# Kernel tuning notes

Hardware: AMD Instinct MI355X
Metric: run time of the kernel (lower is better)

The kernel has to match this reference:

```python
import jax, jax.numpy as jnp
import numpy as np

B, C_IN, C_HID, H, W = 4, 512, 512, 64, 64


def setup_inputs() -> dict:
    key = jax.random.key(0)
    ks = jax.random.split(key, 9)
    s_in = 1.0 / np.sqrt(C_IN)
    s_hid = 1.0 / np.sqrt(C_HID)
    return {
        "inp": jax.random.normal(ks[0], (B, C_IN, H, W), dtype=jnp.float32),
        "Wk": jax.random.normal(ks[1], (C_HID, C_IN), dtype=jnp.float32) * s_in,
        "bk": jax.random.normal(ks[2], (C_HID,), dtype=jnp.float32) * 0.01,
        "Wq": jax.random.normal(ks[3], (C_HID, C_IN), dtype=jnp.float32) * s_in,
        "bq": jax.random.normal(ks[4], (C_HID,), dtype=jnp.float32) * 0.01,
        "Wv": jax.random.normal(ks[5], (C_HID, C_IN), dtype=jnp.float32) * s_in,
        "bv": jax.random.normal(ks[6], (C_HID,), dtype=jnp.float32) * 0.01,
        "Wo": jax.random.normal(ks[7], (C_IN, C_HID), dtype=jnp.float32) * s_hid,
        "bo": jax.random.normal(ks[8], (C_IN,), dtype=jnp.float32) * 0.01,
    }


def reference(inp, Wk, bk, Wq, bq, Wv, bv, Wo, bo):
    b, _, h, w = inp.shape
    n = h * w

    def conv1x1(x, Wt, bias):  # 1x1 conv == per-pixel GEMM
        return jnp.einsum('bchw,oc->bohw', x, Wt) + bias[None, :, None, None]

    k = conv1x1(inp, Wk, bk).reshape(b, C_HID, n)   # [B,Ch,N]
    q = conv1x1(inp, Wq, bq).reshape(b, C_HID, n)
    v = conv1x1(inp, Wv, bv).reshape(b, C_HID, n)

    scale = 1.0 / jnp.sqrt(jnp.asarray(C_HID, dtype=jnp.float32))
    # weight[b,i,j] = <key_i, query_j> / sqrt(Ch); softmax over j (dim=2)
    scores = jnp.einsum('bci,bcj->bij', k, q) * scale  # [B,N,N]
    weight = jax.nn.softmax(scores, axis=2)
    # out[b,c,i] = sum_j weight[b,i,j] * v[b,c,j]
    out = jnp.einsum('bij,bcj->bci', weight, v).reshape(b, C_HID, h, w)
    return conv1x1(out, Wo, bo)  # [B,C_in,H,W]
```

## Files before the change

### kernel.cpp

```cpp
#include <hip/hip_runtime.h>
#include <hip/hip_bf16.h>


typedef __attribute__((ext_vector_type(4))) float f32x4;
typedef __attribute__((ext_vector_type(8))) short short8;
typedef __attribute__((ext_vector_type(4))) short short4v;

#define QSCALE 0.06376639774f
#define FENCE asm volatile("" ::: "memory")
#define SBAR  do { FENCE; __builtin_amdgcn_s_barrier(); FENCE; } while (0)
#define LGKM0 asm volatile("s_waitcnt lgkmcnt(0)" ::: "memory")

__device__ __forceinline__ unsigned short f2bf(float f) {
  unsigned u = __builtin_bit_cast(unsigned, f);
  unsigned r = (u + 0x7FFFu + ((u >> 16) & 1u)) >> 16;
  return (unsigned short)r;
}

__device__ __forceinline__ void gll16(const void* g, void* l) {
  __builtin_amdgcn_global_load_lds((const __attribute__((address_space(1))) void*)g,
                                   (__attribute__((address_space(3))) void*)l, 16, 0, 0);
}

#define MFMA_BF16(d, va, vb) \
  d = __builtin_amdgcn_mfma_f32_16x16x32_bf16(va, vb, d, 0, 0, 0)

__device__ __forceinline__ void gemm256_fine(
    const short* __restrict__ A, int lda,
    const short* __restrict__ B, int ldb,
    int nkt, char* sm, f32x4 (&acc)[8][4]) {
  const int tid = threadIdx.x, w = tid >> 6, lane = tid & 63;
  const int g = lane >> 4, l15 = lane & 15;
  const int wm = w >> 2, wn = w & 3;
  const int swz = (l15 & 7) << 4;
  const int brow = (wn & 1) << 6;
  const char* SAb = sm + (wm << 14);
  const char* SBb = sm + 65536 + ((wn >> 1) << 14);

  auto stage = [&](int mat, int half, int t) {
    if (t >= nkt) return;
    char* dst = sm + mat * 65536 + ((t & 1) << 15) + (half << 14) + (w << 10);
    const short* src = mat ? B : A;
    const int ld = mat ? ldb : lda;
    const char* gs = (const char*)src + ((size_t)(half * 128) * ld + (size_t)t * 64) * 2;
#pragma unroll
    for (int q = 0; q < 2; ++q) {
      int o = (q << 13) | (w << 10) | (lane << 4);
      int row = o >> 7, cb = (o & 127) ^ ((row & 7) << 4);
      gll16(gs + (size_t)row * (ld * 2) + cb, dst + (q << 13));
    }
  };
  auto rdA = [&](short8* a4, int mf0, int ks, int buf) {
    const char* SA = SAb + (buf << 15);
#pragma unroll
    for (int i = 0; i < 4; ++i)
      a4[i] = *(const short8*)(SA + ((mf0 + i) * 16 + l15) * 128 + ((ks * 64 + g * 16) ^ swz));
  };
  auto rdB = [&](short8* b4, int ks, int buf) {
    const char* SB = SBb + (buf << 15);
#pragma unroll
    for (int nf = 0; nf < 4; ++nf)
      b4[nf] = *(const short8*)(SB + (brow + nf * 16 + l15) * 128 + ((ks * 64 + g * 16) ^ swz));
  };
  auto mm = [&](short8* a4, short8* b4, int mf0) {
    __builtin_amdgcn_s_setprio(1);
#pragma unroll
    for (int i = 0; i < 4; ++i)
#pragma unroll
      for (int nf = 0; nf < 4; ++nf)
        MFMA_BF16(acc[mf0 + i][nf], a4[i], b4[nf]);
    __builtin_amdgcn_s_setprio(0);
  };

  stage(1, 0, 0); stage(1, 1, 0); stage(0, 0, 0); stage(0, 1, 0); stage(1, 0, 1);

  for (int T = 0; T < nkt; T += 2) {
    short8 a[8], bb[4];
    asm volatile("s_waitcnt vmcnt(2)" ::: "memory"); SBAR;
    rdA(a, 0, 0, 0); rdB(bb, 0, 0); stage(1, 1, T + 1);
    SBAR; LGKM0; mm(a, bb, 0); SBAR;
    rdA(a + 4, 4, 0, 0); stage(0, 0, T + 1);
    SBAR; LGKM0; mm(a + 4, bb, 4); SBAR;
    rdA(a, 0, 1, 0); rdB(bb, 1, 0); stage(0, 1, T + 1);
    SBAR; LGKM0; mm(a, bb, 0); SBAR;
    rdA(a + 4, 4, 1, 0); stage(1, 0, T + 2);
    SBAR; LGKM0; mm(a + 4, bb, 4); SBAR;
    if (T + 2 < nkt) { asm volatile("s_waitcnt vmcnt(2)" ::: "memory"); }
    else             { asm volatile("s_waitcnt vmcnt(0)" ::: "memory"); }
    SBAR;
    rdA(a, 0, 0, 1); rdB(bb, 0, 1); stage(1, 1, T + 2);
    SBAR; LGKM0; mm(a, bb, 0); SBAR;
    rdA(a + 4, 4, 0, 1); stage(0, 0, T + 2);
    SBAR; LGKM0; mm(a + 4, bb, 4); SBAR;
    rdA(a, 0, 1, 1); rdB(bb, 1, 1); stage(0, 1, T + 2);
    SBAR; LGKM0; mm(a, bb, 0); SBAR;
    rdA(a + 4, 4, 1, 1); stage(1, 0, T + 3);
    SBAR; LGKM0; mm(a + 4, bb, 4); SBAR;
  }
}

#define BOUNCE256_WRITE(smp, row, colb, val) \
  *(short*)((smp) + (row) * 512 + (((colb)) ^ (((row) & 7) << 4))) = (val)

__device__ __forceinline__ void bounce256_flush(const char* smp, short* gbase,
                                                int pitch ) {
  const int tid = threadIdx.x;
  SBAR;
#pragma unroll
  for (int it = 0; it < 16; ++it) {
    int row = (tid >> 5) + it * 16;
    short8 v = *(const short8*)(smp + row * 512 + (((tid & 31) * 16) ^ ((row & 7) << 4)));
    *(short8*)(gbase + (size_t)row * pitch + (tid & 31) * 8) = v;
  }
}

__global__ __launch_bounds__(256) void cvt_w_kernel(
    const float* __restrict__ wk, const float* __restrict__ wq,
    const float* __restrict__ wv, const float* __restrict__ wo,
    short* __restrict__ o) {
  int z = blockIdx.y;
  const float* s = (z == 0) ? wk : (z == 1) ? wq : (z == 2) ? wv : wo;
  int i = blockIdx.x * 256 + threadIdx.x;
  float4 f = ((const float4*)s)[i];
  short4v v;
  v[0] = (short)f2bf(f.x); v[1] = (short)f2bf(f.y);
  v[2] = (short)f2bf(f.z); v[3] = (short)f2bf(f.w);
  if (z < 3) {
    *(short4v*)(o + z * 262144 + i * 4) = v;
  } else {
    int idx = i * 4, co = idx >> 9, cc = idx & 511;
    short* base = o + 786432 + co * 1024 + cc;
    *(short4v*)base = v;
    *(short4v*)(base + 512) = v;
  }
}

__global__ __launch_bounds__(256) void transpose_x_kernel(
    const float* __restrict__ inp, short* __restrict__ xt) {
  __shared__ float t[32][33];
  int tx = threadIdx.x, ty = threadIdx.y;
  int n0 = blockIdx.x * 32, c0 = blockIdx.y * 32, b = blockIdx.z;
  const float* src = inp + ((size_t)(b * 512 + c0)) * 4096 + n0;
#pragma unroll
  for (int r = 0; r < 4; ++r) t[ty + r * 8][tx] = src[(ty + r * 8) * 4096 + tx];
  __syncthreads();
  short* dst = xt + ((size_t)((b << 12) + n0)) * 512 + c0;
#pragma unroll
  for (int r = 0; r < 4; ++r) dst[(ty + r * 8) * 512 + tx] = (short)f2bf(t[tx][ty + r * 8]);
}

__global__ __launch_bounds__(512, 2) void kqv256_kernel(
    const short* __restrict__ xt,
    const short* __restrict__ wk, const short* __restrict__ wq, const short* __restrict__ wv,
    const float* __restrict__ bk, const float* __restrict__ bq, const float* __restrict__ bv,
    short* __restrict__ kt, short* __restrict__ qt, short* __restrict__ vc) {
  extern __shared__ char sm[];
  const int bid = blockIdx.x;
  const int xcd = bid & 7, s = bid >> 3;
  const int pg = s / 6, t = s % 6;
  const int panel = pg * 8 + xcd;
  const int z = (t < 4) ? (t >> 1) : 2;
  const short *A, *B;
  int arow0, brow0;
  if (z < 2) {
    arow0 = panel * 256; brow0 = (t & 1) * 256;
    A = xt + (size_t)arow0 * 512;
    B = ((z == 0) ? wk : wq) + (size_t)brow0 * 512;
  } else {
    arow0 = (t - 4) * 256; brow0 = panel * 256;
    A = wv + (size_t)arow0 * 512;
    B = xt + (size_t)brow0 * 512;
  }
  f32x4 acc[8][4] = {};
  gemm256_fine(A, 512, B, 512, 8, sm, acc);
  const int tid = threadIdx.x, w = tid >> 6, lane = tid & 63;
  const int gq = lane >> 4, l15 = lane & 15;
  const int wm = w >> 2, wn = w & 3;
#pragma unroll
  for (int mf = 0; mf < 8; ++mf)
#pragma unroll
    for (int nf = 0; nf < 4; ++nf)
#pragma unroll
      for (int r = 0; r < 4; ++r) {
        int row = wm * 128 + mf * 16 + gq * 4 + r;
        int col = wn * 64 + nf * 16 + l15;
        float v = acc[mf][nf][r], val;
        if (z == 0)      val = (v + bk[brow0 + col]) * QSCALE;
        else if (z == 1) val = v + bq[brow0 + col];
        else             val = v + bv[arow0 + row];
        BOUNCE256_WRITE(sm, row, col * 2, (short)f2bf(val));
      }
  short* gbase; int pitch;
  if (z == 0)      { gbase = kt + (size_t)arow0 * 512 + brow0; pitch = 512; }
  else if (z == 1) { gbase = qt + (size_t)arow0 * 512 + brow0; pitch = 512; }
  else             { gbase = vc + (size_t)arow0 * 16384 + brow0; pitch = 16384; }
  bounce256_flush(sm, gbase, pitch);
}

__global__ __launch_bounds__(512, 2) void gemm_s256_kernel(
    const short* __restrict__ kt, const short* __restrict__ qt,
    short* __restrict__ P, float* __restrict__ Lpart) {
  extern __shared__ char sm[];
  const int bid = blockIdx.x;
  const int xcd = bid & 7, s = bid >> 3;
  const int b = xcd >> 1, h = xcd & 1;
  const int jt0 = (s & 7) * 256, i0 = (s >> 3) * 256;
  const short* A = kt + ((size_t)(b << 12) + i0) * 512;
  const short* B = qt + ((size_t)((b << 12) + h * 2048 + jt0)) * 512;
  f32x4 acc[8][4] = {};
  gemm256_fine(A, 512, B, 512, 8, sm, acc);
  const int tid = threadIdx.x, w = tid >> 6, lane = tid & 63;
  const int gq = lane >> 4, l15 = lane & 15;
  const int wm = w >> 2, wn = w & 3;
  const int jp = (h * 2048 + jt0 + wn * 64) >> 6;
  float* Lp = Lpart + (((size_t)b * 64 + jp) << 12) + i0 + wm * 128;
#pragma unroll
  for (int mf = 0; mf < 8; ++mf) {
    float psum[4] = {0.f, 0.f, 0.f, 0.f};
#pragma unroll
    for (int nf = 0; nf < 4; ++nf)
#pragma unroll
      for (int r = 0; r < 4; ++r) {
        float p = exp2f(acc[mf][nf][r]);
        psum[r] += p;
        int row = wm * 128 + mf * 16 + gq * 4 + r;
        int colb = (wn * 64 + nf * 16 + l15) * 2;
        BOUNCE256_WRITE(sm, row, colb, (short)f2bf(p));
      }
#pragma unroll
    for (int r = 0; r < 4; ++r) {
      float ss = psum[r];
      ss += __shfl_xor(ss, 1); ss += __shfl_xor(ss, 2);
      ss += __shfl_xor(ss, 4); ss += __shfl_xor(ss, 8);
      if (l15 == 0) Lp[mf * 16 + gq * 4 + r] = ss;
    }
  }
  short* gbase = P + (size_t)h * 33554432 + ((size_t)((b << 12) + i0)) * 2048 + jt0;
  bounce256_flush(sm, gbase, 2048);
}

__global__ __launch_bounds__(512, 2) void gemm_pv256_kernel(
    const short* __restrict__ P, const short* __restrict__ vc,
    short* __restrict__ otab) {
  extern __shared__ char sm[];
  const int bid = blockIdx.x;
  const int xcd = bid & 7, s = bid >> 3;
  const int b = xcd >> 1, h = xcd & 1;
  const int c0 = (s & 1) * 256, i0 = (s >> 1) * 256;
  const short* A = P + (size_t)h * 33554432 + ((size_t)((b << 12) + i0)) * 2048;
  const short* B = vc + (size_t)c0 * 16384 + (b << 12) + h * 2048;
  f32x4 acc[8][4] = {};
  gemm256_fine(A, 2048, B, 16384, 32, sm, acc);
  const int tid = threadIdx.x, w = tid >> 6, lane = tid & 63;
  const int gq = lane >> 4, l15 = lane & 15;
  const int wm = w >> 2, wn = w & 3;
#pragma unroll
  for (int mf = 0; mf < 8; ++mf)
#pragma unroll
    for (int nf = 0; nf < 4; ++nf)
#pragma unroll
      for (int r = 0; r < 4; ++r) {
        int row = wm * 128 + mf * 16 + gq * 4 + r;
        int colb = (wn * 64 + nf * 16 + l15) * 2;
        BOUNCE256_WRITE(sm, row, colb, (short)f2bf(acc[mf][nf][r]));
      }
  short* gbase = otab + ((size_t)((b << 12) + i0)) * 1024 + h * 512 + c0;
  bounce256_flush(sm, gbase, 1024);
}

__global__ __launch_bounds__(256) void lred_kernel(
    const float* __restrict__ Lpart, float* __restrict__ linv) {
  int i = blockIdx.x * 256 + threadIdx.x;
  int b = i >> 12;
  float s = 0.f;
#pragma unroll 8
  for (int jp = 0; jp < 64; ++jp) s += Lpart[(((size_t)b * 64 + jp) << 12) + (i & 4095)];
  linv[i] = 1.0f / s;
}

__global__ __launch_bounds__(512, 2) void out256_kernel(
    const short* __restrict__ wdup, const short* __restrict__ otab,
    const float* __restrict__ bo, const float* __restrict__ linv,
    float* __restrict__ out) {
  extern __shared__ char sm[];
  const int bid = blockIdx.x;
  const int xcd = bid & 7, nt = bid >> 3;
  const int b = xcd >> 1, cot = xcd & 1;
  const int arow0 = cot * 256;
  const int bn0 = nt * 256;
  const short* A = wdup + (size_t)arow0 * 1024;
  const short* B = otab + ((size_t)((b << 12) + bn0)) * 1024;
  f32x4 acc[8][4] = {};
  gemm256_fine(A, 1024, B, 1024, 16, sm, acc);
  const int tid = threadIdx.x, w = tid >> 6, lane = tid & 63;
  const int gq = lane >> 4, l15 = lane & 15;
  const int wm = w >> 2, wn = w & 3;
#pragma unroll
  for (int mf = 0; mf < 8; ++mf) {
    int co = arow0 + wm * 128 + mf * 16 + gq * 4;
#pragma unroll
    for (int nf = 0; nf < 4; ++nf) {
      int nl = bn0 + wn * 64 + nf * 16 + l15;
      float li = linv[(b << 12) + nl];
#pragma unroll
      for (int r = 0; r < 4; ++r)
        out[((size_t)(b * 512 + co + r) << 12) + nl] = acc[mf][nf][r] * li + bo[co + r];
    }
  }
}

extern "C" void kernel_launch(void* const* d_in, const int* in_sizes, int n_in,
                              void* d_out, int out_size, void* d_ws, size_t ws_size,
                              hipStream_t stream) {
  const float* inp = (const float*)d_in[0];
  const float* Wk = (const float*)d_in[1];
  const float* bk = (const float*)d_in[2];
  const float* Wq = (const float*)d_in[3];
  const float* bq = (const float*)d_in[4];
  const float* Wv = (const float*)d_in[5];
  const float* bv = (const float*)d_in[6];
  const float* Wo = (const float*)d_in[7];
  const float* bo = (const float*)d_in[8];
  float* out = (float*)d_out;
  char* ws = (char*)d_ws;
  const size_t MB = 1048576;
  short* kt    = (short*)(ws);
  short* qt    = (short*)(ws + 16 * MB);
  short* vc    = (short*)(ws + 32 * MB);
  short* wb    = (short*)(ws + 48 * MB);
  short* xt    = (short*)(ws + 51 * MB);
  float* Lpart = (float*)(ws + 51 * MB);
  float* linv  = (float*)(ws + 55 * MB);
  short* P     = (short*)(ws + 67 * MB);
  short* otab  = (short*)(ws + 195 * MB);

  (void)in_sizes; (void)n_in; (void)out_size; (void)ws_size;

  hipFuncSetAttribute((const void*)kqv256_kernel,
                      hipFuncAttributeMaxDynamicSharedMemorySize, 131072);
  hipFuncSetAttribute((const void*)gemm_s256_kernel,
                      hipFuncAttributeMaxDynamicSharedMemorySize, 131072);
  hipFuncSetAttribute((const void*)gemm_pv256_kernel,
                      hipFuncAttributeMaxDynamicSharedMemorySize, 131072);
  hipFuncSetAttribute((const void*)out256_kernel,
                      hipFuncAttributeMaxDynamicSharedMemorySize, 131072);

  cvt_w_kernel<<<dim3(256, 4), 256, 0, stream>>>(Wk, Wq, Wv, Wo, wb);
  transpose_x_kernel<<<dim3(128, 16, 4), dim3(32, 8, 1), 0, stream>>>(inp, xt);
  kqv256_kernel<<<384, 512, 131072, stream>>>(
      xt, wb, wb + 262144, wb + 524288, bk, bq, bv, kt, qt, vc);
  gemm_s256_kernel<<<1024, 512, 131072, stream>>>(kt, qt, P, Lpart);
  gemm_pv256_kernel<<<256, 512, 131072, stream>>>(P, vc, otab);
  lred_kernel<<<64, 256, 0, stream>>>(Lpart, linv);
  out256_kernel<<<128, 512, 131072, stream>>>(wb + 786432, otab, bo, linv, out);
}
```

Measured before the change: 279.7 us.

## Make score GEMM persistent over four j-tiles with a hand-scheduled LDS pipeline

After: 477.5 us. 1.71x slower.

```diff
diff --git a/kernel.cpp b/kernel.cpp
--- a/kernel.cpp
+++ b/kernel.cpp
@@ -114,6 +114,46 @@
   }
 }
 
+__device__ __forceinline__ void gemm_core(const short* __restrict__ A, int lda,
+                                          const short* __restrict__ B, int ldb,
+                                          int nk, short* lds, f32x4 (&acc)[4][4]) {
+  const int tid = threadIdx.x, w = tid >> 6, lane = tid & 63;
+  const int g = lane >> 4, l15 = lane & 15;
+  const int wr = w >> 1, wc = w & 1;
+  const int rsub = lane >> 2, slot = lane & 3;
+  char* la = (char*)lds;
+  char* lb = (char*)(lds + 128 * 32);
+  for (int ki = 0; ki < nk; ++ki) {
+    const int k0 = ki * 32;
+    __syncthreads();
+#pragma unroll
+    for (int q = 0; q < 2; ++q) {
+      int qq = w * 2 + q;
+      int row = qq * 16 + rsub;
+      int soff = ((slot ^ (row & 3)) * 16);
+      gll16((const char*)(A + (size_t)row * lda + k0) + soff, la + qq * 1024);
+      gll16((const char*)(B + (size_t)row * ldb + k0) + soff, lb + qq * 1024);
+    }
+    __syncthreads();
+    short8 am[4], bn[4];
+#pragma unroll
+    for (int m = 0; m < 4; ++m) {
+      int row = wr * 64 + m * 16 + l15;
+      am[m] = *(const short8*)(la + row * 64 + ((g * 16) ^ ((l15 & 3) << 4)));
+    }
+#pragma unroll
+    for (int n = 0; n < 4; ++n) {
+      int row = wc * 64 + n * 16 + l15;
+      bn[n] = *(const short8*)(lb + row * 64 + ((g * 16) ^ ((l15 & 3) << 4)));
+    }
+#pragma unroll
+    for (int m = 0; m < 4; ++m)
+#pragma unroll
+      for (int n = 0; n < 4; ++n)
+        MFMA_BF16(acc[m][n], am[m], bn[n]);
+  }
+}
+
 __global__ __launch_bounds__(256) void cvt_w_kernel(
     const float* __restrict__ wk, const float* __restrict__ wq,
     const float* __restrict__ wv, const float* __restrict__ wo,
@@ -203,40 +243,134 @@
   extern __shared__ char sm[];
   const int bid = blockIdx.x;
   const int xcd = bid & 7, s = bid >> 3;
-  const int b = xcd >> 1, h = xcd & 1;
-  const int jt0 = (s & 7) * 256, i0 = (s >> 3) * 256;
-  const short* A = kt + ((size_t)(b << 12) + i0) * 512;
-  const short* B = qt + ((size_t)((b << 12) + h * 2048 + jt0)) * 512;
-  f32x4 acc[8][4] = {};
-  gemm256_fine(A, 512, B, 512, 8, sm, acc);
-  const int tid = threadIdx.x, w = tid >> 6, lane = tid & 63;
-  const int gq = lane >> 4, l15 = lane & 15;
+  const int b = xcd >> 1, ih = xcd & 1;
+  const int jg = s >> 3, il = s & 7;
+  const int i0 = (ih * 8 + il) * 256;
+  const int tid = threadIdx.x, w = tid >> 6, lane = tid & 63;
+  const int g = lane >> 4, l15 = lane & 15;
   const int wm = w >> 2, wn = w & 3;
-  const int jp = (h * 2048 + jt0 + wn * 64) >> 6;
-  float* Lp = Lpart + (((size_t)b * 64 + jp) << 12) + i0 + wm * 128;
-#pragma unroll
-  for (int mf = 0; mf < 8; ++mf) {
-    float psum[4] = {0.f, 0.f, 0.f, 0.f};
+  const int swz = (l15 & 7) << 4;
+  const int brow = (wn & 1) << 6;
+  const char* SAb = sm + (wm << 14);
+  const char* SBb = sm + 65536 + ((wn >> 1) << 14);
+  char* smB = sm + 65536;
+
+  const short* A = kt + ((size_t)((b << 12) + i0)) * 512;
+  const short* Bp = qt + ((size_t)((b << 12) + jg * 1024)) * 512;
+
+  auto stage = [&](int mat, int half, int t) {
+    if (t >= 8) return;
+    char* dst = sm + mat * 65536 + ((t & 1) << 15) + (half << 14) + (w << 10);
+    const short* src = mat ? Bp : A;
+    const char* gs = (const char*)src + ((size_t)(half * 128) * 512 + (size_t)t * 64) * 2;
+#pragma unroll
+    for (int q = 0; q < 2; ++q) {
+      int o = (q << 13) | (w << 10) | (lane << 4);
+      int row = o >> 7, cb = (o & 127) ^ ((row & 7) << 4);
+      gll16(gs + (size_t)row * 1024 + cb, dst + (q << 13));
+    }
+  };
+  auto rdA = [&](short8* a4, int mf0, int ks, int buf) {
+    const char* SA = SAb + (buf << 15);
+#pragma unroll
+    for (int i = 0; i < 4; ++i)
+      a4[i] = *(const short8*)(SA + ((mf0 + i) * 16 + l15) * 128 + ((ks * 64 + g * 16) ^ swz));
+  };
+  auto rdB = [&](short8* b4, int ks, int buf) {
+    const char* SB = SBb + (buf << 15);
 #pragma unroll
     for (int nf = 0; nf < 4; ++nf)
+      b4[nf] = *(const short8*)(SB + (brow + nf * 16 + l15) * 128 + ((ks * 64 + g * 16) ^ swz));
+  };
+
+  stage(1, 0, 0); stage(1, 1, 0); stage(0, 0, 0); stage(0, 1, 0); stage(1, 0, 1);
+
+  for (int jt = 0; jt < 4; ++jt) {
+    f32x4 acc[8][4] = {};
+    auto mm = [&](short8* a4, short8* b4, int mf0) {
+      __builtin_amdgcn_s_setprio(1);
+#pragma unroll
+      for (int i = 0; i < 4; ++i)
+#pragma unroll
+        for (int nf = 0; nf < 4; ++nf)
+          MFMA_BF16(acc[mf0 + i][nf], a4[i], b4[nf]);
+      __builtin_amdgcn_s_setprio(0);
+    };
+    for (int T = 0; T < 8; T += 2) {
+      short8 a[8], bb[4];
+      asm volatile("s_waitcnt vmcnt(2)" ::: "memory"); SBAR;
+      rdA(a, 0, 0, 0); rdB(bb, 0, 0); stage(1, 1, T + 1);
+      SBAR; LGKM0; mm(a, bb, 0); SBAR;
+      rdA(a + 4, 4, 0, 0); stage(0, 0, T + 1);
+      SBAR; LGKM0; mm(a + 4, bb, 4); SBAR;
+      rdA(a, 0, 1, 0); rdB(bb, 1, 0); stage(0, 1, T + 1);
+      SBAR; LGKM0; mm(a, bb, 0); SBAR;
+      rdA(a + 4, 4, 1, 0); stage(1, 0, T + 2);
+      SBAR; LGKM0; mm(a + 4, bb, 4); SBAR;
+      if (T + 2 < 8) { asm volatile("s_waitcnt vmcnt(2)" ::: "memory"); }
+      else           { asm volatile("s_waitcnt vmcnt(0)" ::: "memory"); }
+      SBAR;
+      rdA(a, 0, 0, 1); rdB(bb, 0, 1); stage(1, 1, T + 2);
+      SBAR; LGKM0; mm(a, bb, 0); SBAR;
+      rdA(a + 4, 4, 0, 1); stage(0, 0, T + 2);
+      SBAR; LGKM0; mm(a + 4, bb, 4); SBAR;
+      rdA(a, 0, 1, 1); rdB(bb, 1, 1); stage(0, 1, T + 2);
+      SBAR; LGKM0; mm(a, bb, 0); SBAR;
+      rdA(a + 4, 4, 1, 1); stage(1, 0, T + 3);
+      SBAR; LGKM0; mm(a + 4, bb, 4); SBAR;
+    }
+    const int jglob = jg * 1024 + jt * 256;
+    const int h = jglob >> 11, jl = jglob & 2047;
+    if (jt < 3) { stage(0, 0, 0); stage(0, 1, 0); }
+    float psum[8][4];
+#pragma unroll
+    for (int mf = 0; mf < 8; ++mf)
+#pragma unroll
+      for (int r = 0; r < 4; ++r) psum[mf][r] = 0.f;
+#pragma unroll
+    for (int hf = 0; hf < 2; ++hf) {
+      SBAR;
+      if (wm == hf) {
+#pragma unroll
+        for (int mf = 0; mf < 8; ++mf)
+#pragma unroll
+          for (int nf = 0; nf < 4; ++nf)
+#pragma unroll
+            for (int r = 0; r < 4; ++r) {
+              float p = exp2f(acc[mf][nf][r]);
+              psum[mf][r] += p;
+              int row = mf * 16 + g * 4 + r;
+              int colb = (wn * 64 + nf * 16 + l15) * 2;
+              *(short*)(smB + row * 512 + (colb ^ ((row & 7) << 4))) = (short)f2bf(p);
+            }
+      }
+      SBAR;
+      short* gbase = P + (size_t)h * 33554432 +
+                     ((size_t)((b << 12) + i0 + hf * 128)) * 2048 + jl;
+#pragma unroll
+      for (int it = 0; it < 8; ++it) {
+        int row = (tid >> 5) + it * 16;
+        short8 v = *(const short8*)(smB + row * 512 +
+                                    (((tid & 31) * 16) ^ ((row & 7) << 4)));
+        *(short8*)(gbase + (size_t)row * 2048 + (tid & 31) * 8) = v;
+      }
+    }
+    const int jp = (jglob + wn * 64) >> 6;
+    float* Lp = Lpart + (((size_t)b * 64 + jp) << 12) + i0 + wm * 128;
+#pragma unroll
+    for (int mf = 0; mf < 8; ++mf)
 #pragma unroll
       for (int r = 0; r < 4; ++r) {
-        float p = exp2f(acc[mf][nf][r]);
-        psum[r] += p;
-        int row = wm * 128 + mf * 16 + gq * 4 + r;
-        int colb = (wn * 64 + nf * 16 + l15) * 2;
-        BOUNCE256_WRITE(sm, row, colb, (short)f2bf(p));
+        float ss = psum[mf][r];
+        ss += __shfl_xor(ss, 1); ss += __shfl_xor(ss, 2);
+        ss += __shfl_xor(ss, 4); ss += __shfl_xor(ss, 8);
+        if (l15 == 0) Lp[mf * 16 + g * 4 + r] = ss;
       }
-#pragma unroll
-    for (int r = 0; r < 4; ++r) {
-      float ss = psum[r];
-      ss += __shfl_xor(ss, 1); ss += __shfl_xor(ss, 2);
-      ss += __shfl_xor(ss, 4); ss += __shfl_xor(ss, 8);
-      if (l15 == 0) Lp[mf * 16 + gq * 4 + r] = ss;
-    }
-  }
-  short* gbase = P + (size_t)h * 33554432 + ((size_t)((b << 12) + i0)) * 2048 + jt0;
-  bounce256_flush(sm, gbase, 2048);
+    if (jt < 3) {
+      Bp = qt + ((size_t)((b << 12) + jglob + 256)) * 512;
+      stage(1, 0, 0); stage(1, 1, 0); stage(1, 0, 1);
+    }
+  }
 }
 
 __global__ __launch_bounds__(512, 2) void gemm_pv256_kernel(
@@ -349,7 +483,7 @@
   transpose_x_kernel<<<dim3(128, 16, 4), dim3(32, 8, 1), 0, stream>>>(inp, xt);
   kqv256_kernel<<<384, 512, 131072, stream>>>(
       xt, wb, wb + 262144, wb + 524288, bk, bq, bv, kt, qt, vc);
-  gemm_s256_kernel<<<1024, 512, 131072, stream>>>(kt, qt, P, Lpart);
+  gemm_s256_kernel<<<256, 512, 131072, stream>>>(kt, qt, P, Lpart);
   gemm_pv256_kernel<<<256, 512, 131072, stream>>>(P, vc, otab);
   lred_kernel<<<64, 256, 0, stream>>>(Lpart, linv);
   out256_kernel<<<128, 512, 131072, stream>>>(wb + 786432, otab, bo, linv, out);
```

## Replace fine-grained GEMM schedule with register double-buffered pipeline; drop LDS epilogue bounce

Applied to the files above, without the earlier changes.

After: 283.0 us. No clear change (+1.2%).

```diff
diff --git a/kernel.cpp b/kernel.cpp
--- a/kernel.cpp
+++ b/kernel.cpp
@@ -25,7 +25,7 @@
 #define MFMA_BF16(d, va, vb) \
   d = __builtin_amdgcn_mfma_f32_16x16x32_bf16(va, vb, d, 0, 0, 0)
 
-__device__ __forceinline__ void gemm256_fine(
+__device__ __forceinline__ void gemm256_pipe(
     const short* __restrict__ A, int lda,
     const short* __restrict__ B, int ldb,
     int nkt, char* sm, f32x4 (&acc)[8][4]) {
@@ -37,80 +37,63 @@
   const char* SAb = sm + (wm << 14);
   const char* SBb = sm + 65536 + ((wn >> 1) << 14);
 
-  auto stage = [&](int mat, int half, int t) {
+  auto stageT = [&](int t) {
     if (t >= nkt) return;
-    char* dst = sm + mat * 65536 + ((t & 1) << 15) + (half << 14) + (w << 10);
-    const short* src = mat ? B : A;
-    const int ld = mat ? ldb : lda;
-    const char* gs = (const char*)src + ((size_t)(half * 128) * ld + (size_t)t * 64) * 2;
-#pragma unroll
-    for (int q = 0; q < 2; ++q) {
-      int o = (q << 13) | (w << 10) | (lane << 4);
-      int row = o >> 7, cb = (o & 127) ^ ((row & 7) << 4);
-      gll16(gs + (size_t)row * (ld * 2) + cb, dst + (q << 13));
+    const int buf = t & 1;
+#pragma unroll
+    for (int mat = 0; mat < 2; ++mat) {
+      const short* src = mat ? B : A;
+      const int ld = mat ? ldb : lda;
+#pragma unroll
+      for (int half = 0; half < 2; ++half) {
+        char* dst = sm + mat * 65536 + (buf << 15) + (half << 14) + (w << 10);
+        const char* gs = (const char*)src + ((size_t)(half * 128) * ld + (size_t)t * 64) * 2;
+#pragma unroll
+        for (int q = 0; q < 2; ++q) {
+          int o = (q << 13) | (w << 10) | (lane << 4);
+          int row = o >> 7, cb = (o & 127) ^ ((row & 7) << 4);
+          gll16(gs + (size_t)row * (ld * 2) + cb, dst + (q << 13));
+        }
+      }
     }
   };
-  auto rdA = [&](short8* a4, int mf0, int ks, int buf) {
+  auto rdSlice = [&](short8* af, short8* bf, int ks, int buf) {
     const char* SA = SAb + (buf << 15);
-#pragma unroll
-    for (int i = 0; i < 4; ++i)
-      a4[i] = *(const short8*)(SA + ((mf0 + i) * 16 + l15) * 128 + ((ks * 64 + g * 16) ^ swz));
+    const char* SB = SBb + (buf << 15);
+#pragma unroll
+    for (int i = 0; i < 8; ++i)
+      af[i] = *(const short8*)(SA + (i * 16 + l15) * 128 + ((ks * 64 + g * 16) ^ swz));
+#pragma unroll
+    for (int nf = 0; nf < 4; ++nf)
+      bf[nf] = *(const short8*)(SB + (brow + nf * 16 + l15) * 128 + ((ks * 64 + g * 16) ^ swz));
   };
-  auto rdB = [&](short8* b4, int ks, int buf) {
-    const char* SB = SBb + (buf << 15);
-#pragma unroll
-    for (int nf = 0; nf < 4; ++nf)
-      b4[nf] = *(const short8*)(SB + (brow + nf * 16 + l15) * 128 + ((ks * 64 + g * 16) ^ swz));
-  };
-  auto mm = [&](short8* a4, short8* b4, int mf0) {
+  auto mmAll = [&](short8* af, short8* bf) {
     __builtin_amdgcn_s_setprio(1);
 #pragma unroll
-    for (int i = 0; i < 4; ++i)
+    for (int i = 0; i < 8; ++i)
 #pragma unroll
       for (int nf = 0; nf < 4; ++nf)
-        MFMA_BF16(acc[mf0 + i][nf], a4[i], b4[nf]);
+        MFMA_BF16(acc[i][nf], af[i], bf[nf]);
     __builtin_amdgcn_s_setprio(0);
   };
 
-  stage(1, 0, 0); stage(1, 1, 0); stage(0, 0, 0); stage(0, 1, 0); stage(1, 0, 1);
-
-  for (int T = 0; T < nkt; T += 2) {
-    short8 a[8], bb[4];
-    asm volatile("s_waitcnt vmcnt(2)" ::: "memory"); SBAR;
-    rdA(a, 0, 0, 0); rdB(bb, 0, 0); stage(1, 1, T + 1);
-    SBAR; LGKM0; mm(a, bb, 0); SBAR;
-    rdA(a + 4, 4, 0, 0); stage(0, 0, T + 1);
-    SBAR; LGKM0; mm(a + 4, bb, 4); SBAR;
-    rdA(a, 0, 1, 0); rdB(bb, 1, 0); stage(0, 1, T + 1);
-    SBAR; LGKM0; mm(a, bb, 0); SBAR;
-    rdA(a + 4, 4, 1, 0); stage(1, 0, T + 2);
-    SBAR; LGKM0; mm(a + 4, bb, 4); SBAR;
-    if (T + 2 < nkt) { asm volatile("s_waitcnt vmcnt(2)" ::: "memory"); }
-    else             { asm volatile("s_waitcnt vmcnt(0)" ::: "memory"); }
-    SBAR;
-    rdA(a, 0, 0, 1); rdB(bb, 0, 1); stage(1, 1, T + 2);
-    SBAR; LGKM0; mm(a, bb, 0); SBAR;
-    rdA(a + 4, 4, 0, 1); stage(0, 0, T + 2);
-    SBAR; LGKM0; mm(a + 4, bb, 4); SBAR;
-    rdA(a, 0, 1, 1); rdB(bb, 1, 1); stage(0, 1, T + 2);
-    SBAR; LGKM0; mm(a, bb, 0); SBAR;
-    rdA(a + 4, 4, 1, 1); stage(1, 0, T + 3);
-    SBAR; LGKM0; mm(a + 4, bb, 4); SBAR;
-  }
-}
-
-#define BOUNCE256_WRITE(smp, row, colb, val) \
-  *(short*)((smp) + (row) * 512 + (((colb)) ^ (((row) & 7) << 4))) = (val)
-
-__device__ __forceinline__ void bounce256_flush(const char* smp, short* gbase,
-                                                int pitch ) {
-  const int tid = threadIdx.x;
-  SBAR;
-#pragma unroll
-  for (int it = 0; it < 16; ++it) {
-    int row = (tid >> 5) + it * 16;
-    short8 v = *(const short8*)(smp + row * 512 + (((tid & 31) * 16) ^ ((row & 7) << 4)));
-    *(short8*)(gbase + (size_t)row * pitch + (tid & 31) * 8) = v;
+  stageT(0); stageT(1);
+  asm volatile("s_waitcnt vmcnt(8)" ::: "memory"); SBAR;
+  short8 aX[8], bX[4], aY[8], bY[4];
+  rdSlice(aX, bX, 0, 0);
+  for (int T = 0; T < nkt; ++T) {
+    const int buf = T & 1;
+    rdSlice(aY, bY, 1, buf);
+    mmAll(aX, bX);
+    LGKM0; SBAR;
+    stageT(T + 2);
+    if (T + 1 < nkt) {
+      if (T + 2 < nkt) asm volatile("s_waitcnt vmcnt(8)" ::: "memory");
+      else             asm volatile("s_waitcnt vmcnt(0)" ::: "memory");
+      SBAR;
+      rdSlice(aX, bX, 0, buf ^ 1);
+    }
+    mmAll(aY, bY);
   }
 }
 
@@ -172,7 +155,7 @@
     B = xt + (size_t)brow0 * 512;
   }
   f32x4 acc[8][4] = {};
-  gemm256_fine(A, 512, B, 512, 8, sm, acc);
+  gemm256_pipe(A, 512, B, 512, 8, sm, acc);
   const int tid = threadIdx.x, w = tid >> 6, lane = tid & 63;
   const int gq = lane >> 4, l15 = lane & 15;
   const int wm = w >> 2, wn = w & 3;
@@ -184,17 +167,14 @@
       for (int r = 0; r < 4; ++r) {
         int row = wm * 128 + mf * 16 + gq * 4 + r;
         int col = wn * 64 + nf * 16 + l15;
-        float v = acc[mf][nf][r], val;
-        if (z == 0)      val = (v + bk[brow0 + col]) * QSCALE;
-        else if (z == 1) val = v + bq[brow0 + col];
-        else             val = v + bv[arow0 + row];
-        BOUNCE256_WRITE(sm, row, col * 2, (short)f2bf(val));
+        float v = acc[mf][nf][r];
+        if (z == 0)      kt[(size_t)(arow0 + row) * 512 + brow0 + col] =
+                           (short)f2bf((v + bk[brow0 + col]) * QSCALE);
+        else if (z == 1) qt[(size_t)(arow0 + row) * 512 + brow0 + col] =
+                           (short)f2bf(v + bq[brow0 + col]);
+        else             vc[(size_t)(arow0 + row) * 16384 + brow0 + col] =
+                           (short)f2bf(v + bv[arow0 + row]);
       }
-  short* gbase; int pitch;
-  if (z == 0)      { gbase = kt + (size_t)arow0 * 512 + brow0; pitch = 512; }
-  else if (z == 1) { gbase = qt + (size_t)arow0 * 512 + brow0; pitch = 512; }
-  else             { gbase = vc + (size_t)arow0 * 16384 + brow0; pitch = 16384; }
-  bounce256_flush(sm, gbase, pitch);
 }
 
 __global__ __launch_bounds__(512, 2) void gemm_s256_kernel(
@@ -208,35 +188,38 @@
   const short* A = kt + ((size_t)(b << 12) + i0) * 512;
   const short* B = qt + ((size_t)((b << 12) + h * 2048 + jt0)) * 512;
   f32x4 acc[8][4] = {};
-  gemm256_fine(A, 512, B, 512, 8, sm, acc);
+  gemm256_pipe(A, 512, B, 512, 8, sm, acc);
   const int tid = threadIdx.x, w = tid >> 6, lane = tid & 63;
   const int gq = lane >> 4, l15 = lane & 15;
   const int wm = w >> 2, wn = w & 3;
+  short* Pb = P + (size_t)h * 33554432 +
+              ((size_t)((b << 12) + i0 + wm * 128)) * 2048 + jt0 + wn * 64;
+  float psum[8][4];
+#pragma unroll
+  for (int mf = 0; mf < 8; ++mf)
+#pragma unroll
+    for (int r = 0; r < 4; ++r) psum[mf][r] = 0.f;
+#pragma unroll
+  for (int mf = 0; mf < 8; ++mf)
+#pragma unroll
+    for (int nf = 0; nf < 4; ++nf)
+#pragma unroll
+      for (int r = 0; r < 4; ++r) {
+        float p = exp2f(acc[mf][nf][r]);
+        psum[mf][r] += p;
+        Pb[(size_t)(mf * 16 + gq * 4 + r) * 2048 + nf * 16 + l15] = (short)f2bf(p);
+      }
   const int jp = (h * 2048 + jt0 + wn * 64) >> 6;
   float* Lp = Lpart + (((size_t)b * 64 + jp) << 12) + i0 + wm * 128;
 #pragma unroll
-  for (int mf = 0; mf < 8; ++mf) {
-    float psum[4] = {0.f, 0.f, 0.f, 0.f};
-#pragma unroll
-    for (int nf = 0; nf < 4; ++nf)
-#pragma unroll
-      for (int r = 0; r < 4; ++r) {
-        float p = exp2f(acc[mf][nf][r]);
-        psum[r] += p;
-        int row = wm * 128 + mf * 16 + gq * 4 + r;
-        int colb = (wn * 64 + nf * 16 + l15) * 2;
-        BOUNCE256_WRITE(sm, row, colb, (short)f2bf(p));
-      }
+  for (int mf = 0; mf < 8; ++mf)
 #pragma unroll
     for (int r = 0; r < 4; ++r) {
-      float ss = psum[r];
+      float ss = psum[mf][r];
       ss += __shfl_xor(ss, 1); ss += __shfl_xor(ss, 2);
       ss += __shfl_xor(ss, 4); ss += __shfl_xor(ss, 8);
       if (l15 == 0) Lp[mf * 16 + gq * 4 + r] = ss;
     }
-  }
-  short* gbase = P + (size_t)h * 33554432 + ((size_t)((b << 12) + i0)) * 2048 + jt0;
-  bounce256_flush(sm, gbase, 2048);
 }
 
 __global__ __launch_bounds__(512, 2) void gemm_pv256_kernel(
@@ -250,22 +233,19 @@
   const short* A = P + (size_t)h * 33554432 + ((size_t)((b << 12) + i0)) * 2048;
   const short* B = vc + (size_t)c0 * 16384 + (b << 12) + h * 2048;
   f32x4 acc[8][4] = {};
-  gemm256_fine(A, 2048, B, 16384, 32, sm, acc);
+  gemm256_pipe(A, 2048, B, 16384, 32, sm, acc);
   const int tid = threadIdx.x, w = tid >> 6, lane = tid & 63;
   const int gq = lane >> 4, l15 = lane & 15;
   const int wm = w >> 2, wn = w & 3;
+  short* Ob = otab + ((size_t)((b << 12) + i0 + wm * 128)) * 1024 + h * 512 + c0 + wn * 64;
 #pragma unroll
   for (int mf = 0; mf < 8; ++mf)
 #pragma unroll
     for (int nf = 0; nf < 4; ++nf)
 #pragma unroll
-      for (int r = 0; r < 4; ++r) {
-        int row = wm * 128 + mf * 16 + gq * 4 + r;
-        int colb = (wn * 64 + nf * 16 + l15) * 2;
-        BOUNCE256_WRITE(sm, row, colb, (short)f2bf(acc[mf][nf][r]));
-      }
-  short* gbase = otab + ((size_t)((b << 12) + i0)) * 1024 + h * 512 + c0;
-  bounce256_flush(sm, gbase, 1024);
+      for (int r = 0; r < 4; ++r)
+        Ob[(size_t)(mf * 16 + gq * 4 + r) * 1024 + nf * 16 + l15] =
+            (short)f2bf(acc[mf][nf][r]);
 }
 
 __global__ __launch_bounds__(256) void lred_kernel(
@@ -291,7 +271,7 @@
   const short* A = wdup + (size_t)arow0 * 1024;
   const short* B = otab + ((size_t)((b << 12) + bn0)) * 1024;
   f32x4 acc[8][4] = {};
-  gemm256_fine(A, 1024, B, 1024, 16, sm, acc);
+  gemm256_pipe(A, 1024, B, 1024, 16, sm, acc);
   const int tid = threadIdx.x, w = tid >> 6, lane = tid & 63;
   const int gq = lane >> 4, l15 = lane & 15;
   const int wm = w >> 2, wn = w & 3;
```
